# Kernel tuning notes

Hardware: AMD Instinct MI355X
Metric: run time of the kernel (lower is better)

## Reference

```python
import jax, jax.numpy as jnp
import numpy as np

B, T, F, H = 256, 32, 128, 128
NUM_FILTERS, KH, KW, NUM_CLASSES = 64, 2, 2, 2
FLAT = NUM_FILTERS * (T - KH + 1) * (2 * F - KW + 1)  # 64*31*255 = 505920


def setup_inputs() -> dict:
    key = jax.random.key(0)
    ks = jax.random.split(key, 12)
    inp = {
        "X_nume": jax.random.normal(ks[0], (B, T, F), jnp.float32),
        "att_W": jax.random.uniform(ks[1], (F, H), jnp.float32),
        "att_U": jax.random.uniform(ks[2], (F, H), jnp.float32),
        "att_V": jax.random.uniform(ks[3], (H, 1), jnp.float32),
        "conv_w": jax.random.normal(ks[4], (NUM_FILTERS, 1, KH, KW), jnp.float32) * 0.5,
        "conv_b": jax.random.normal(ks[5], (NUM_FILTERS,), jnp.float32) * 0.1,
        "w1": jax.random.normal(ks[6], (FLAT, 256), jnp.float32) * (1.0 / np.sqrt(FLAT)),
        "b1": jnp.zeros((256,), jnp.float32),
        "w2": jax.random.normal(ks[7], (256, 32), jnp.float32) * (1.0 / np.sqrt(256)),
        "b2": jnp.zeros((32,), jnp.float32),
        "w3": jax.random.normal(ks[8], (32, NUM_CLASSES), jnp.float32) * (1.0 / np.sqrt(32)),
        "b3": jnp.zeros((NUM_CLASSES,), jnp.float32),
    }
    return inp


def reference(X_nume, att_W, att_U, att_V, conv_w, conv_b, w1, b1, w2, b2, w3, b3):
    X = X_nume  # [B, T, F]
    # --- additive attention, fully batched (replaces O(T^2) python loops) ---
    xw = jnp.einsum("btf,fh->bth", X, att_W)  # query proj [B,T,H]
    xu = jnp.einsum("btf,fh->bth", X, att_U)  # key proj   [B,T,H]
    # e[b,i,j] = V^T tanh(x_i W + x_j U)
    scores = jnp.squeeze(jnp.tanh(xw[:, :, None, :] + xu[:, None, :, :]) @ att_V, -1)  # [B,T,T]
    alpha = jax.nn.softmax(scores, axis=-1)  # softmax over j (includes diagonal)
    # context excludes j == i (original skips j == index AFTER softmax)
    mask = 1.0 - jnp.eye(T, dtype=X.dtype)
    c = jnp.einsum("bij,bjf->bif", alpha * mask, X)  # [B,T,F]
    feat = jnp.concatenate([X, c], axis=-1)  # [B,T,2F]
    # --- conv ---
    conv_in = feat[:, None, :, :]  # [B,1,T,2F]
    conv = jax.lax.conv_general_dilated(
        conv_in, conv_w, window_strides=(1, 1), padding="VALID",
        dimension_numbers=("NCHW", "OIHW", "NCHW"))
    conv = jax.nn.relu(conv + conv_b[None, :, None, None])  # [B,64,T-1,2F-1]
    # --- MLP head ---
    flat = conv.reshape(conv.shape[0], -1)
    h = jax.nn.relu(flat @ w1 + b1)
    h = jax.nn.relu(h @ w2 + b2)
    return h @ w3 + b3
```

## Files before the change

### kernel.cpp

```cpp
#include <hip/hip_runtime.h>
#include <hip/hip_bf16.h>

#define B_ 256
#define T_ 32
#define F_ 128
#define H_ 128
#define NF 64
#define OH 31
#define OW 255
#define POS_TOTAL (OH*OW)
#define N1 256
#define KT 248

typedef __attribute__((ext_vector_type(8))) short bf16x8;
typedef __attribute__((ext_vector_type(4))) float f32x4;

__device__ __forceinline__ unsigned int cvtpk(float lo, float hi) {
    unsigned int r;
    asm("v_cvt_pk_bf16_f32 %0, %1, %2" : "=v"(r) : "v"(lo), "v"(hi));
    return r;
}

__global__ __launch_bounds__(256) void k_attn(
    const float* __restrict__ X, const float* __restrict__ W,
    const float* __restrict__ U, const float* __restrict__ V,
    float* __restrict__ featL)
{
    __shared__ float Xs[T_][F_];
    __shared__ float xw[T_][H_];
    __shared__ float xu[T_][H_];
    __shared__ float sc[T_][T_];
    __shared__ float Vs[H_];

    const int b = blockIdx.x;
    const int t = threadIdx.x;
    const float* Xb = X + (size_t)b * T_ * F_;

    for (int idx = t; idx < T_*F_; idx += 256) ((float*)Xs)[idx] = Xb[idx];
    if (t < H_) Vs[t] = V[t];
    __syncthreads();

    {
        const int h = t & 127, half = t >> 7;
        float aw[16], au[16];
        #pragma unroll
        for (int r = 0; r < 16; r++) { aw[r] = 0.f; au[r] = 0.f; }
        for (int f = 0; f < F_; f++) {
            const float wv = W[f*H_ + h];
            const float uv = U[f*H_ + h];
            #pragma unroll
            for (int r = 0; r < 16; r++) {
                const float xv = Xs[half*16 + r][f];
                aw[r] += xv * wv;
                au[r] += xv * uv;
            }
        }
        #pragma unroll
        for (int r = 0; r < 16; r++) {
            xw[half*16 + r][h] = aw[r];
            xu[half*16 + r][h] = au[r];
        }
    }
    __syncthreads();

    {
        const int i = t >> 3;
        const int j0 = (t & 7) * 4;
        float s0 = 0.f, s1 = 0.f, s2 = 0.f, s3 = 0.f;
        for (int h = 0; h < H_; h++) {
            const float xwv = xw[i][h];
            const float vv  = Vs[h];
            s0 += tanhf(xwv + xu[j0+0][h]) * vv;
            s1 += tanhf(xwv + xu[j0+1][h]) * vv;
            s2 += tanhf(xwv + xu[j0+2][h]) * vv;
            s3 += tanhf(xwv + xu[j0+3][h]) * vv;
        }
        sc[i][j0+0] = s0; sc[i][j0+1] = s1; sc[i][j0+2] = s2; sc[i][j0+3] = s3;
    }
    __syncthreads();

    if (t < T_) {
        float m = -1e30f;
        #pragma unroll
        for (int j = 0; j < T_; j++) m = fmaxf(m, sc[t][j]);
        float sum = 0.f;
        #pragma unroll
        for (int j = 0; j < T_; j++) sum += expf(sc[t][j] - m);
        const float inv = 1.f / sum;
        #pragma unroll
        for (int j = 0; j < T_; j++) {
            const float a = expf(sc[t][j] - m) * inv;
            sc[t][j] = (j == t) ? 0.f : a;
        }
    }
    __syncthreads();

    for (int idx = t; idx < T_*F_; idx += 256) {
        const int row = idx >> 7, f = idx & 127;
        float acc = 0.f;
        #pragma unroll
        for (int j = 0; j < T_; j++) acc += sc[row][j] * Xs[j][f];
        float* fr = featL + (size_t)b*8192 + row*256;
        fr[f]       = Xs[row][f];
        fr[128 + f] = acc;
    }
}

__global__ __launch_bounds__(256) void k_tr(
    const float* __restrict__ src, float* __restrict__ dst)
{
    __shared__ float tile[32][33];
    const int rc0 = blockIdx.x * 32;
    const int b0  = blockIdx.y * 32;
    const int tx = threadIdx.x & 31;
    const int ty = threadIdx.x >> 5;
    #pragma unroll
    for (int r = 0; r < 32; r += 8)
        tile[ty + r][tx] = src[(size_t)(b0 + ty + r)*8192 + rc0 + tx];
    __syncthreads();
    #pragma unroll
    for (int r = 0; r < 32; r += 8)
        dst[(size_t)(rc0 + ty + r)*256 + b0 + tx] = tile[tx][ty + r];
}

__global__ __launch_bounds__(512, 2) void k_gemm1(
    const float* __restrict__ featT, const float* __restrict__ cw,
    const float* __restrict__ cb, const float* __restrict__ w1,
    float* __restrict__ partial)
{
    __shared__ unsigned short As[2][256*64];
    __shared__ float cwL[256];
    __shared__ float cbL[64];

    const int t  = threadIdx.x;
    const int kt = blockIdx.x;
    const int y  = kt >> 3;
    const int x0 = (kt & 7) * 32;

    if (t < 256) cwL[t] = cw[t];
    if (t < 64)  cbL[t] = cb[t];

    const int rm = t & 255;
    const int ph = t >> 8;
    const int lane = t & 63, wid = t >> 6;
    const int wn = wid * 32;
    const int fr = lane & 15, fq = lane >> 4;

    f32x4 acc[16][2];
    #pragma unroll
    for (int i = 0; i < 16; i++) {
        acc[i][0] = (f32x4){0.f, 0.f, 0.f, 0.f};
        acc[i][1] = (f32x4){0.f, 0.f, 0.f, 0.f};
    }

    float topv[17], botv[17];
    #pragma unroll
    for (int i = 0; i < 17; i++) {
        int xc = x0 + ph*16 + i; if (xc > 255) xc = 255;
        topv[i] = featT[((size_t)(y*256 + xc))*256 + rm];
        botv[i] = featT[((size_t)((y+1)*256 + xc))*256 + rm];
    }

    int poff[8];
    #pragma unroll
    for (int j = 0; j < 8; j++) {
        int xc = x0 + fq*8 + j; if (xc > 254) xc = 254;
        poff[j] = (y*255 + xc)*N1 + wn + fr;
    }

    float wv[2][2][8];

#define WLOAD(S)                                                               \
    {                                                                          \
        _Pragma("unroll")                                                      \
        for (int kc = 0; kc < 2; kc++) {                                       \
            const float* wf_ = w1 + (size_t)(2*(S) + kc) * (POS_TOTAL*N1);     \
            _Pragma("unroll")                                                  \
            for (int ng = 0; ng < 2; ng++)                                     \
                _Pragma("unroll")                                              \
                for (int j = 0; j < 8; j++)                                    \
                    wv[kc][ng][j] = wf_[poff[j] + ng*16];                      \
        }                                                                      \
    }

#define STAGE(BUF, S)                                                          \
    {                                                                          \
        _Pragma("unroll")                                                      \
        for (int fl = 0; fl < 2; fl++) {                                       \
            const int f_ = 2*(S) + fl;                                         \
            const float4 cc_ = *(const float4*)&cwL[f_*4];                     \
            const float cbv_ = cbL[f_];                                        \
            unsigned int pk_[4];                                               \
            _Pragma("unroll")                                                  \
            for (int i2 = 0; i2 < 8; i2++) {                                   \
                const int i0 = 2*i2, i1 = 2*i2 + 1;                            \
                float v0_ = topv[i0]*cc_.x + topv[i0+1]*cc_.y                  \
                          + botv[i0]*cc_.z + botv[i0+1]*cc_.w + cbv_;          \
                float v1_ = topv[i1]*cc_.x + topv[i1+1]*cc_.y                  \
                          + botv[i1]*cc_.z + botv[i1+1]*cc_.w + cbv_;          \
                v0_ = (x0 + ph*16 + i0 < 255) ? fmaxf(v0_, 0.f) : 0.f;         \
                v1_ = (x0 + ph*16 + i1 < 255) ? fmaxf(v1_, 0.f) : 0.f;         \
                pk_[i2 & 3] = cvtpk(v0_, v1_);                                 \
                if ((i2 & 3) == 3) {                                           \
                    const int kb_ = fl*4 + ph*2 + (i2 >> 2);                   \
                    *(uint4*)&As[BUF][rm*64 + ((kb_ ^ (rm & 7))*8)]            \
                        = *(uint4*)&pk_[0];                                    \
                }                                                              \
            }                                                                  \
        }                                                                      \
    }

    WLOAD(0);
    __syncthreads();
    STAGE(0, 0);
    asm volatile("s_waitcnt lgkmcnt(0)" ::: "memory");
    __builtin_amdgcn_s_barrier();

    #pragma unroll 1
    for (int s = 0; s < 32; s++) {
        const int cur = s & 1;

        bf16x8 bf[2][2];
        #pragma unroll
        for (int kc = 0; kc < 2; kc++)
            #pragma unroll
            for (int ng = 0; ng < 2; ng++) {
                unsigned int* bu = (unsigned int*)&bf[kc][ng];
                #pragma unroll
                for (int q = 0; q < 4; q++)
                    bu[q] = cvtpk(wv[kc][ng][2*q], wv[kc][ng][2*q+1]);
            }

        if (s < 31) WLOAD(s + 1);

        __builtin_amdgcn_s_setprio(1);
        #pragma unroll
        for (int kc = 0; kc < 2; kc++) {
            const int sw = ((kc*4 + fq) ^ (fr & 7)) * 8;
            #pragma unroll
            for (int mg = 0; mg < 16; mg++) {
                const bf16x8 af =
                    *(const bf16x8*)&As[cur][(mg*16 + fr)*64 + sw];
                acc[mg][0] = __builtin_amdgcn_mfma_f32_16x16x32_bf16(
                    af, bf[kc][0], acc[mg][0], 0, 0, 0);
                acc[mg][1] = __builtin_amdgcn_mfma_f32_16x16x32_bf16(
                    af, bf[kc][1], acc[mg][1], 0, 0, 0);
            }
        }
        __builtin_amdgcn_s_setprio(0);

        if (s < 31) STAGE(cur ^ 1, s + 1);
        asm volatile("s_waitcnt lgkmcnt(0)" ::: "memory");
        __builtin_amdgcn_s_barrier();
    }

    float* pp = partial + (size_t)kt * (256*N1);
    #pragma unroll
    for (int mg = 0; mg < 16; mg++)
        #pragma unroll
        for (int ng = 0; ng < 2; ng++) {
            const int col = wn + ng*16 + fr;
            #pragma unroll
            for (int j = 0; j < 4; j++) {
                const int row = mg*16 + fq*4 + j;
                pp[(size_t)row*N1 + col] = acc[mg][ng][j];
            }
        }
#undef WLOAD
#undef STAGE
}

__global__ __launch_bounds__(256) void k_head(
    const float* __restrict__ partial,
    const float* __restrict__ b1, const float* __restrict__ w2,
    const float* __restrict__ b2, const float* __restrict__ w3,
    const float* __restrict__ b3, float* __restrict__ out)
{
    __shared__ float h1s[256];
    __shared__ float h2s[32];
    const int b = blockIdx.x, t = threadIdx.x;

    const float* pb = partial + (size_t)b*N1 + t;
    float s0 = 0.f, s1 = 0.f, s2 = 0.f, s3 = 0.f;
    #pragma unroll 2
    for (int kt = 0; kt < KT; kt += 4) {
        s0 += pb[(size_t)(kt+0)*65536];
        s1 += pb[(size_t)(kt+1)*65536];
        s2 += pb[(size_t)(kt+2)*65536];
        s3 += pb[(size_t)(kt+3)*65536];
    }
    h1s[t] = fmaxf(b1[t] + ((s0+s1)+(s2+s3)), 0.f);
    __syncthreads();

    if (t < 32) {
        float s2v = b2[t];
        for (int i = 0; i < 256; i++) s2v += h1s[i] * w2[i*32 + t];
        h2s[t] = fmaxf(s2v, 0.f);
    }
    __syncthreads();

    if (t < 2) {
        float s3v = b3[t];
        #pragma unroll
        for (int i = 0; i < 32; i++) s3v += h2s[i] * w3[i*2 + t];
        out[b*2 + t] = s3v;
    }
}

extern "C" void kernel_launch(void* const* d_in, const int* in_sizes, int n_in,
                              void* d_out, int out_size, void* d_ws, size_t ws_size,
                              hipStream_t stream) {
    const float* X    = (const float*)d_in[0];
    const float* attW = (const float*)d_in[1];
    const float* attU = (const float*)d_in[2];
    const float* attV = (const float*)d_in[3];
    const float* cw   = (const float*)d_in[4];
    const float* cb   = (const float*)d_in[5];
    const float* w1   = (const float*)d_in[6];
    const float* b1   = (const float*)d_in[7];
    const float* w2   = (const float*)d_in[8];
    const float* b2   = (const float*)d_in[9];
    const float* w3   = (const float*)d_in[10];
    const float* b3   = (const float*)d_in[11];
    float* out = (float*)d_out;

    float* featL   = (float*)d_ws;
    float* featT   = (float*)((char*)d_ws + (8u<<20));
    float* partial = (float*)((char*)d_ws + (16u<<20));

    k_attn <<<dim3(B_),       dim3(256), 0, stream>>>(X, attW, attU, attV, featL);
    k_tr   <<<dim3(256, 8),   dim3(256), 0, stream>>>(featL, featT);
    k_gemm1<<<dim3(KT),       dim3(512), 0, stream>>>(featT, cw, cb, w1, partial);
    k_head <<<dim3(B_),       dim3(256), 0, stream>>>(partial, b1, w2, b2, w3, b3, out);
}
```

Measured before the change: 260.7 us.

## Split gemm1 N dimension across two blocks and pack conv inputs as bf16

The GEMM1 grid gains a second dimension that splits the 256 output columns into two halves, so each block and wave handles half the N width with fewer accumulators. Conv input rows are held as packed bf16 pairs instead of fp32, and launch bounds rise to four blocks per CU. Together these cut register pressure so more blocks can be resident to hide the latency of the w1 stream, and the doubled block count fills more CUs. In exchange, the conv/ReLU staging and the A-tile LDS writes are now done twice (once per N half), and the conv inputs lose precision by being rounded to bf16 before the convolution.

```diff
diff --git a/kernel.cpp b/kernel.cpp
--- a/kernel.cpp
+++ b/kernel.cpp
@@ -20,6 +20,9 @@
     asm("v_cvt_pk_bf16_f32 %0, %1, %2" : "=v"(r) : "v"(lo), "v"(hi));
     return r;
 }
+#define PLO(u) __uint_as_float((u) << 16)
+#define PHI(u) __uint_as_float((u) & 0xffff0000u)
+#define PAT(arr, i) (((i) & 1) ? PHI(arr[(i) >> 1]) : PLO(arr[(i) >> 1]))
 
 __global__ __launch_bounds__(256) void k_attn(
     const float* __restrict__ X, const float* __restrict__ W,
@@ -123,7 +126,7 @@
         dst[(size_t)(rc0 + ty + r)*256 + b0 + tx] = tile[tx][ty + r];
 }
 
-__global__ __launch_bounds__(512, 2) void k_gemm1(
+__global__ __launch_bounds__(512, 4) void k_gemm1(
     const float* __restrict__ featT, const float* __restrict__ cw,
     const float* __restrict__ cb, const float* __restrict__ w1,
     float* __restrict__ partial)
@@ -133,7 +136,8 @@
     __shared__ float cbL[64];
 
     const int t  = threadIdx.x;
-    const int kt = blockIdx.x;
+    const int nt = blockIdx.x;
+    const int kt = blockIdx.y;
     const int y  = kt >> 3;
     const int x0 = (kt & 7) * 32;
 
@@ -143,44 +147,38 @@
     const int rm = t & 255;
     const int ph = t >> 8;
     const int lane = t & 63, wid = t >> 6;
-    const int wn = wid * 32;
+    const int wn = nt*128 + wid*16;
     const int fr = lane & 15, fq = lane >> 4;
 
-    f32x4 acc[16][2];
-    #pragma unroll
-    for (int i = 0; i < 16; i++) {
-        acc[i][0] = (f32x4){0.f, 0.f, 0.f, 0.f};
-        acc[i][1] = (f32x4){0.f, 0.f, 0.f, 0.f};
-    }
-
-    float topv[17], botv[17];
-    #pragma unroll
-    for (int i = 0; i < 17; i++) {
-        int xc = x0 + ph*16 + i; if (xc > 255) xc = 255;
-        topv[i] = featT[((size_t)(y*256 + xc))*256 + rm];
-        botv[i] = featT[((size_t)((y+1)*256 + xc))*256 + rm];
-    }
-
-    int poff[8];
+    f32x4 acc[16];
+    #pragma unroll
+    for (int i = 0; i < 16; i++) acc[i] = (f32x4){0.f, 0.f, 0.f, 0.f};
+
+    unsigned int tp[9], bp[9];
+    #pragma unroll
+    for (int q = 0; q < 9; q++) {
+        int xa = x0 + ph*16 + 2*q;     if (xa > 255) xa = 255;
+        int xb = x0 + ph*16 + 2*q + 1; if (xb > 255) xb = 255;
+        tp[q] = cvtpk(featT[((size_t)(y*256 + xa))*256 + rm],
+                      featT[((size_t)(y*256 + xb))*256 + rm]);
+        bp[q] = cvtpk(featT[((size_t)((y+1)*256 + xa))*256 + rm],
+                      featT[((size_t)((y+1)*256 + xb))*256 + rm]);
+    }
+
+    int boff[8];
     #pragma unroll
     for (int j = 0; j < 8; j++) {
         int xc = x0 + fq*8 + j; if (xc > 254) xc = 254;
-        poff[j] = (y*255 + xc)*N1 + wn + fr;
-    }
-
-    float wv[2][2][8];
-
-#define WLOAD(S)                                                               \
+        boff[j] = (y*255 + xc)*N1 + wn + fr;
+    }
+
+    float wv[2][8];
+
+#define WLOADH(KC, F)                                                          \
     {                                                                          \
+        const float* wf_ = w1 + (size_t)(F) * (POS_TOTAL*N1);                  \
         _Pragma("unroll")                                                      \
-        for (int kc = 0; kc < 2; kc++) {                                       \
-            const float* wf_ = w1 + (size_t)(2*(S) + kc) * (POS_TOTAL*N1);     \
-            _Pragma("unroll")                                                  \
-            for (int ng = 0; ng < 2; ng++)                                     \
-                _Pragma("unroll")                                              \
-                for (int j = 0; j < 8; j++)                                    \
-                    wv[kc][ng][j] = wf_[poff[j] + ng*16];                      \
-        }                                                                      \
+        for (int j = 0; j < 8; j++) wv[KC][j] = wf_[boff[j]];                  \
     }
 
 #define STAGE(BUF, S)                                                          \
@@ -194,10 +192,10 @@
             _Pragma("unroll")                                                  \
             for (int i2 = 0; i2 < 8; i2++) {                                   \
                 const int i0 = 2*i2, i1 = 2*i2 + 1;                            \
-                float v0_ = topv[i0]*cc_.x + topv[i0+1]*cc_.y                  \
-                          + botv[i0]*cc_.z + botv[i0+1]*cc_.w + cbv_;          \
-                float v1_ = topv[i1]*cc_.x + topv[i1+1]*cc_.y                  \
-                          + botv[i1]*cc_.z + botv[i1+1]*cc_.w + cbv_;          \
+                float v0_ = PAT(tp,i0)*cc_.x + PAT(tp,i0+1)*cc_.y              \
+                          + PAT(bp,i0)*cc_.z + PAT(bp,i0+1)*cc_.w + cbv_;      \
+                float v1_ = PAT(tp,i1)*cc_.x + PAT(tp,i1+1)*cc_.y              \
+                          + PAT(bp,i1)*cc_.z + PAT(bp,i1+1)*cc_.w + cbv_;      \
                 v0_ = (x0 + ph*16 + i0 < 255) ? fmaxf(v0_, 0.f) : 0.f;         \
                 v1_ = (x0 + ph*16 + i1 < 255) ? fmaxf(v1_, 0.f) : 0.f;         \
                 pk_[i2 & 3] = cvtpk(v0_, v1_);                                 \
@@ -210,7 +208,8 @@
         }                                                                      \
     }
 
-    WLOAD(0);
+    WLOADH(0, 0);
+    WLOADH(1, 1);
     __syncthreads();
     STAGE(0, 0);
     asm volatile("s_waitcnt lgkmcnt(0)" ::: "memory");
@@ -220,34 +219,40 @@
     for (int s = 0; s < 32; s++) {
         const int cur = s & 1;
 
-        bf16x8 bf[2][2];
-        #pragma unroll
-        for (int kc = 0; kc < 2; kc++)
-            #pragma unroll
-            for (int ng = 0; ng < 2; ng++) {
-                unsigned int* bu = (unsigned int*)&bf[kc][ng];
-                #pragma unroll
-                for (int q = 0; q < 4; q++)
-                    bu[q] = cvtpk(wv[kc][ng][2*q], wv[kc][ng][2*q+1]);
-            }
-
-        if (s < 31) WLOAD(s + 1);
-
-        __builtin_amdgcn_s_setprio(1);
-        #pragma unroll
-        for (int kc = 0; kc < 2; kc++) {
-            const int sw = ((kc*4 + fq) ^ (fr & 7)) * 8;
+        {
+            bf16x8 bf0;
+            unsigned int* bu = (unsigned int*)&bf0;
+            #pragma unroll
+            for (int q = 0; q < 4; q++) bu[q] = cvtpk(wv[0][2*q], wv[0][2*q+1]);
+            if (s < 31) WLOADH(0, 2*(s+1));
+            __builtin_amdgcn_s_setprio(1);
             #pragma unroll
             for (int mg = 0; mg < 16; mg++) {
+                const int sw = ((fq) ^ (fr & 7)) * 8;
                 const bf16x8 af =
                     *(const bf16x8*)&As[cur][(mg*16 + fr)*64 + sw];
-                acc[mg][0] = __builtin_amdgcn_mfma_f32_16x16x32_bf16(
-                    af, bf[kc][0], acc[mg][0], 0, 0, 0);
-                acc[mg][1] = __builtin_amdgcn_mfma_f32_16x16x32_bf16(
-                    af, bf[kc][1], acc[mg][1], 0, 0, 0);
+                acc[mg] = __builtin_amdgcn_mfma_f32_16x16x32_bf16(
+                    af, bf0, acc[mg], 0, 0, 0);
             }
-        }
-        __builtin_amdgcn_s_setprio(0);
+            __builtin_amdgcn_s_setprio(0);
+        }
+        {
+            bf16x8 bf1;
+            unsigned int* bu = (unsigned int*)&bf1;
+            #pragma unroll
+            for (int q = 0; q < 4; q++) bu[q] = cvtpk(wv[1][2*q], wv[1][2*q+1]);
+            if (s < 31) WLOADH(1, 2*(s+1) + 1);
+            __builtin_amdgcn_s_setprio(1);
+            #pragma unroll
+            for (int mg = 0; mg < 16; mg++) {
+                const int sw = ((4 + fq) ^ (fr & 7)) * 8;
+                const bf16x8 af =
+                    *(const bf16x8*)&As[cur][(mg*16 + fr)*64 + sw];
+                acc[mg] = __builtin_amdgcn_mfma_f32_16x16x32_bf16(
+                    af, bf1, acc[mg], 0, 0, 0);
+            }
+            __builtin_amdgcn_s_setprio(0);
+        }
 
         if (s < 31) STAGE(cur ^ 1, s + 1);
         asm volatile("s_waitcnt lgkmcnt(0)" ::: "memory");
@@ -256,17 +261,15 @@
 
     float* pp = partial + (size_t)kt * (256*N1);
     #pragma unroll
-    for (int mg = 0; mg < 16; mg++)
-        #pragma unroll
-        for (int ng = 0; ng < 2; ng++) {
-            const int col = wn + ng*16 + fr;
-            #pragma unroll
-            for (int j = 0; j < 4; j++) {
-                const int row = mg*16 + fq*4 + j;
-                pp[(size_t)row*N1 + col] = acc[mg][ng][j];
-            }
-        }
-#undef WLOAD
+    for (int mg = 0; mg < 16; mg++) {
+        const int col = wn + fr;
+        #pragma unroll
+        for (int j = 0; j < 4; j++) {
+            const int row = mg*16 + fq*4 + j;
+            pp[(size_t)row*N1 + col] = acc[mg][j];
+        }
+    }
+#undef WLOADH
 #undef STAGE
 }
 
@@ -330,6 +333,6 @@
 
     k_attn <<<dim3(B_),       dim3(256), 0, stream>>>(X, attW, attU, attV, featL);
     k_tr   <<<dim3(256, 8),   dim3(256), 0, stream>>>(featL, featT);
-    k_gemm1<<<dim3(KT),       dim3(512), 0, stream>>>(featT, cw, cb, w1, partial);
+    k_gemm1<<<dim3(2, KT),    dim3(512), 0, stream>>>(featT, cw, cb, w1, partial);
     k_head <<<dim3(B_),       dim3(256), 0, stream>>>(partial, b1, w2, b2, w3, b3, out);
 }
```

Measured after the change: 644.1 us. 147% more time.
